# Optimization experiments

Hardware: AMD Instinct MI355X
Metric: run time of the kernel (lower is better)

The kernel has to match this reference:

```python
import jax, jax.numpy as jnp
import numpy as np

NUM_NODES = 50000
HIDDEN = 128
NUM_REL = 8
NUM_EDGES = 600000


def setup_inputs() -> dict:
    key = jax.random.key(0)
    ks = jax.random.split(key, 10)
    s = 1.0 / np.sqrt(HIDDEN)
    return {
        "edge_index": jax.random.randint(ks[0], (2, NUM_EDGES), 0, NUM_NODES, dtype=jnp.int32),
        "edge_type": jax.random.randint(ks[1], (NUM_EDGES,), 0, NUM_REL, dtype=jnp.int32),
        "node_emb": jax.random.normal(ks[2], (NUM_NODES, HIDDEN), jnp.float32),
        "W1": jax.random.normal(ks[3], (NUM_REL, HIDDEN, HIDDEN), jnp.float32) * s,
        "root1": jax.random.normal(ks[4], (HIDDEN, HIDDEN), jnp.float32) * s,
        "b1": jnp.zeros((HIDDEN,), jnp.float32),
        "W2": jax.random.normal(ks[5], (NUM_REL, HIDDEN, HIDDEN), jnp.float32) * s,
        "root2": jax.random.normal(ks[6], (HIDDEN, HIDDEN), jnp.float32) * s,
        "b2": jnp.zeros((HIDDEN,), jnp.float32),
    }


def rgcn_layer(x, W, root, bias, src, dst, rel):
    # PyG RGCNConv: per-relation MEAN aggregation of neighbor features,
    # transformed by relation weight, plus root transform and bias.
    N = x.shape[0]
    R = W.shape[0]
    # transform node features by every relation weight: [N, R, F]
    xw = jnp.einsum('nd,rdf->nrf', x, W)
    # per-(dst, relation) in-edge counts for mean normalization
    cnt = jnp.zeros((N, R), x.dtype).at[dst, rel].add(1.0)
    inv = 1.0 / jnp.maximum(cnt, 1.0)
    # per-edge message, normalized by destination's per-relation degree
    msg = xw[src, rel] * inv[dst, rel][:, None]  # [E, F]
    agg = jnp.zeros((N, W.shape[2]), x.dtype).at[dst].add(msg)
    return agg + x @ root + bias


def reference(edge_index, edge_type, node_emb, W1, root1, b1, W2, root2, b2):
    src, dst = edge_index[0], edge_index[1]
    h = jax.nn.relu(rgcn_layer(node_emb, W1, root1, b1, src, dst, edge_type))
    out = rgcn_layer(h, W2, root2, b2, src, dst, edge_type)
    return out
```

## Files before the change

### kernel.cpp

```cpp
#include <hip/hip_runtime.h>

#define H 128
#define RREL 8
#define NJ 9
#define MT 32
#define LROW 1160

typedef short bf16x8 __attribute__((ext_vector_type(8)));
typedef float f32x4 __attribute__((ext_vector_type(4)));
typedef unsigned short u16x8 __attribute__((ext_vector_type(8)));

static __device__ __forceinline__ unsigned short f2bf(float f) {
    unsigned int u = __float_as_uint(f);
    unsigned int r = (u + 0x7fffu + ((u >> 16) & 1u)) >> 16;
    return (unsigned short)r;
}
static __device__ __forceinline__ float bf2f(unsigned short u) {
    return __uint_as_float(((unsigned int)u) << 16);
}

__global__ void zero_kernel(int* p, long n) {
    long i = (long)blockIdx.x * blockDim.x + threadIdx.x;
    long stride = (long)gridDim.x * blockDim.x;
    for (; i < n; i += stride) p[i] = 0;
}

__global__ void count_kernel(const int* __restrict__ ei, const int* __restrict__ et,
                             int* __restrict__ cnt, int E) {
    int e = blockIdx.x * 256 + threadIdx.x;
    if (e >= E) return;
    int d = ei[E + e];
    int r = et[e];
    atomicAdd(&cnt[(size_t)d * RREL + r], 1);
}

__global__ void scan_block_kernel(const int* __restrict__ cnt, int* __restrict__ rploc,
                                  int* __restrict__ bsum, int N) {
    __shared__ int s[256];
    int t = threadIdx.x;
    int d = blockIdx.x * 256 + t;
    int v = 0;
    if (d < N) {
#pragma unroll
        for (int r = 0; r < RREL; ++r) v += cnt[(size_t)d * RREL + r];
    }
    s[t] = v;
    __syncthreads();
#pragma unroll
    for (int off = 1; off < 256; off <<= 1) {
        int u = 0;
        if (t >= off) u = s[t - off];
        __syncthreads();
        s[t] += u;
        __syncthreads();
    }
    if (d < N) rploc[d] = s[t] - v;
    if (t == 255) bsum[blockIdx.x] = s[255];
}

__global__ void finalize_kernel(const int* __restrict__ cnt, const int* __restrict__ rploc,
                                const int* __restrict__ bsum, int* __restrict__ rowptr,
                                int* __restrict__ rowptr2, float* __restrict__ inv,
                                int N, int nb) {
    __shared__ int s[256];
    int t = threadIdx.x;
    int v = (t < nb) ? bsum[t] : 0;
    s[t] = v;
    __syncthreads();
#pragma unroll
    for (int off = 1; off < 256; off <<= 1) {
        int u = 0;
        if (t >= off) u = s[t - off];
        __syncthreads();
        s[t] += u;
        __syncthreads();
    }
    int boffB = (blockIdx.x == 0) ? 0 : s[blockIdx.x - 1];
    int d = blockIdx.x * 256 + t;
    if (d >= N) return;
    int rp = rploc[d] + boffB;
    rowptr[d] = rp;
    int run = rp;
#pragma unroll
    for (int r = 0; r < RREL; ++r) {
        int c = cnt[(size_t)d * RREL + r];
        rowptr2[(size_t)d * RREL + r] = run;
        inv[(size_t)d * RREL + r] = 1.0f / (float)max(c, 1);
        run += c;
    }
    if (d == N - 1) rowptr[N] = run;
}

__global__ void fill_kernel(const int* __restrict__ ei, const int* __restrict__ et,
                            int* __restrict__ cursor, const int* __restrict__ rowptr2,
                            int* __restrict__ packed, int E) {
    int e = blockIdx.x * 256 + threadIdx.x;
    if (e >= E) return;
    int d = ei[E + e];
    int r = et[e];
    size_t bin = (size_t)d * RREL + r;
    int pos = rowptr2[bin] + atomicAdd(&cursor[bin], 1);
    packed[pos] = ei[e] | (r << 20);
}

__global__ void wcat_tobf_kernel(const float* __restrict__ W1, const float* __restrict__ r1,
                                 const float* __restrict__ W2, const float* __restrict__ r2,
                                 const float* __restrict__ b1, const float* __restrict__ b2,
                                 unsigned short* __restrict__ WTa1, unsigned short* __restrict__ WTa2,
                                 float* __restrict__ biasP,
                                 const float* __restrict__ x, unsigned short* __restrict__ xb,
                                 long nx) {
    const long per = (long)NJ * H * H;
    const long total = per + 2 * H + nx;
    for (long id = (long)blockIdx.x * 256 + threadIdx.x; id < total; id += (long)gridDim.x * 256) {
        if (id < per) {
            int j = (int)(id / (H * H));
            int fk = (int)(id - (long)j * (H * H));
            int f = fk >> 7, k = fk & 127;
            float v1 = (j < RREL) ? W1[((size_t)j * H + k) * H + f] : r1[(size_t)k * H + f];
            WTa1[id] = f2bf(v1);
            float v2 = (j < RREL) ? W2[((size_t)j * H + k) * H + f] : r2[(size_t)k * H + f];
            WTa2[id] = f2bf(v2);
        } else if (id < per + 2 * H) {
            int c = (int)(id - per);
            biasP[c] = (c < H) ? b1[c] : b2[c - H];
        } else {
            long i = id - per - 2 * H;
            xb[i] = f2bf(x[i]);
        }
    }
}

#define ACC(EE, XV, VV)                                                        \
    do {                                                                       \
        int r_ = ((VV) >> 20) & 7;                                             \
        bool nr_ = (r_ != rcur);                                               \
        float ivc_ = __shfl(ivl, gbase + r_);                                  \
        bool pr_ = (hb + (EE)) < m;                                            \
        u16x8 o_;                                                              \
        _Pragma("unroll")                                                      \
        for (int j = 0; j < 8; ++j) {                                          \
            float xx_ = bf2f((unsigned short)(XV)[j]);                         \
            float t0_ = nr_ ? 0.f : tmp[j];                                    \
            tmp[j] = t0_ + (pr_ ? xx_ : 0.f);                                  \
            o_[j] = f2bf(ivc_ * tmp[j]);                                       \
        }                                                                      \
        *(u16x8*)&rowp[r_ * H + kc] = o_;                                      \
        rcur = r_;                                                             \
    } while (0)

__global__ __launch_bounds__(512) void layer_kernel(const unsigned short* __restrict__ xin,
                                                    const unsigned short* __restrict__ WTa,
                                                    const float* __restrict__ biasP,
                                                    const float* __restrict__ inv,
                                                    const int* __restrict__ rowptr,
                                                    const int* __restrict__ packed,
                                                    float* __restrict__ outf,
                                                    unsigned short* __restrict__ outb,
                                                    int N, int relu) {
    __shared__ __align__(16) unsigned short aggS[MT * LROW];
    const int t = threadIdx.x;
    const int l = t & 63;
    const int w = t >> 6;
    const int g16 = t >> 4;
    const int fl = t & 15;
    const int kc = fl * 8;
    const int gbase = l & 48;
    const int Mbase = blockIdx.x * MT;
    const int d = Mbase + g16;
    const bool valid = d < N;

    unsigned short* rowp = &aggS[g16 * LROW];
    {
        u16x8 z = {0, 0, 0, 0, 0, 0, 0, 0};
#pragma unroll
        for (int c = 0; c < 8; ++c) *(u16x8*)&rowp[(c * 16 + fl) * 8] = z;
        if (valid) {
            *(u16x8*)&rowp[RREL * H + kc] = *(const u16x8*)&xin[(size_t)d * H + kc];
        } else {
            *(u16x8*)&rowp[RREL * H + kc] = z;
        }
    }

    int rp = 0;
    if (valid && fl < 2) rp = rowptr[d + fl];
    float ivl = 0.f;
    if (valid && fl < 8) ivl = inv[(size_t)d * RREL + fl];
    int beg = __shfl(rp, gbase);
    int end = __shfl(rp, gbase + 1);

    if (end > beg) {
        float tmp[8] = {};
        int rcur = 100;
        int idx0 = beg + fl; if (idx0 > end - 1) idx0 = end - 1;
        int pk = packed[idx0];
        for (int i = beg; i < end; i += 16) {
            int ni = i + 16 + fl; if (ni > end - 1) ni = end - 1;
            int pkN = packed[ni];
            int m = end - i;
            if (m > 16) m = 16;
#pragma unroll
            for (int half = 0; half < 2; ++half) {
                const int hb = half * 8;
                int v0 = __shfl(pk, gbase + hb + 0);
                int v1 = __shfl(pk, gbase + hb + 1);
                int v2 = __shfl(pk, gbase + hb + 2);
                int v3 = __shfl(pk, gbase + hb + 3);
                int v4 = __shfl(pk, gbase + hb + 4);
                int v5 = __shfl(pk, gbase + hb + 5);
                int v6 = __shfl(pk, gbase + hb + 6);
                int v7 = __shfl(pk, gbase + hb + 7);
                u16x8 x0 = *(const u16x8*)&xin[(size_t)(v0 & 0xFFFFF) * H + kc];
                u16x8 x1 = *(const u16x8*)&xin[(size_t)(v1 & 0xFFFFF) * H + kc];
                u16x8 x2 = *(const u16x8*)&xin[(size_t)(v2 & 0xFFFFF) * H + kc];
                u16x8 x3 = *(const u16x8*)&xin[(size_t)(v3 & 0xFFFFF) * H + kc];
                u16x8 x4 = *(const u16x8*)&xin[(size_t)(v4 & 0xFFFFF) * H + kc];
                u16x8 x5 = *(const u16x8*)&xin[(size_t)(v5 & 0xFFFFF) * H + kc];
                u16x8 x6 = *(const u16x8*)&xin[(size_t)(v6 & 0xFFFFF) * H + kc];
                u16x8 x7 = *(const u16x8*)&xin[(size_t)(v7 & 0xFFFFF) * H + kc];
                __builtin_amdgcn_sched_barrier(0);
                ACC(0, x0, v0);
                ACC(1, x1, v1);
                ACC(2, x2, v2);
                ACC(3, x3, v3);
                ACC(4, x4, v4);
                ACC(5, x5, v5);
                ACC(6, x6, v6);
                ACC(7, x7, v7);
            }
            pk = pkN;
        }
    }

    __syncthreads();

    const int colb = l & 15, quad = l >> 4;
    const int fcol = w * 16 + colb;
    const f32x4 fz = {0.f, 0.f, 0.f, 0.f};
    f32x4 acc0 = fz, acc1 = fz;
    const unsigned short* arow0 = &aggS[colb * LROW];
    const unsigned short* arow1 = &aggS[(16 + colb) * LROW];
#pragma unroll
    for (int j = 0; j < NJ; ++j) {
#pragma unroll
        for (int ks = 0; ks < 4; ++ks) {
            const int kl = ks * 32 + quad * 8;
            bf16x8 b = *(const bf16x8*)&WTa[((size_t)j * H + fcol) * H + kl];
            bf16x8 a0 = *(const bf16x8*)&arow0[j * H + kl];
            bf16x8 a1 = *(const bf16x8*)&arow1[j * H + kl];
            acc0 = __builtin_amdgcn_mfma_f32_16x16x32_bf16(a0, b, acc0, 0, 0, 0);
            acc1 = __builtin_amdgcn_mfma_f32_16x16x32_bf16(a1, b, acc1, 0, 0, 0);
        }
    }

    __syncthreads();
    float* stg = (float*)aggS;
    const float bcol = biasP[fcol];
#pragma unroll
    for (int i = 0; i < 4; ++i) {
        float v0 = acc0[i] + bcol;
        float v1 = acc1[i] + bcol;
        if (relu) { v0 = fmaxf(v0, 0.f); v1 = fmaxf(v1, 0.f); }
        stg[(quad * 4 + i) * 132 + fcol] = v0;
        stg[(16 + quad * 4 + i) * 132 + fcol] = v1;
    }
    __syncthreads();
    {
        int row = t >> 4;
        int dd = Mbase + row;
        if (dd < N) {
            int c0 = fl * 8;
            f32x4 p0 = *(const f32x4*)&stg[row * 132 + c0];
            f32x4 p1 = *(const f32x4*)&stg[row * 132 + c0 + 4];
            if (outf) {
                *(f32x4*)&outf[(size_t)dd * H + c0] = p0;
                *(f32x4*)&outf[(size_t)dd * H + c0 + 4] = p1;
            } else {
                u16x8 o;
#pragma unroll
                for (int j = 0; j < 4; ++j) { o[j] = f2bf(p0[j]); o[4 + j] = f2bf(p1[j]); }
                *(u16x8*)&outb[(size_t)dd * H + c0] = o;
            }
        }
    }
}

extern "C" void kernel_launch(void* const* d_in, const int* in_sizes, int n_in,
                              void* d_out, int out_size, void* d_ws, size_t ws_size,
                              hipStream_t stream) {
    const int* edge_index = (const int*)d_in[0];
    const int* edge_type  = (const int*)d_in[1];
    const float* node_emb = (const float*)d_in[2];
    const float* W1    = (const float*)d_in[3];
    const float* root1 = (const float*)d_in[4];
    const float* b1    = (const float*)d_in[5];
    const float* W2    = (const float*)d_in[6];
    const float* root2 = (const float*)d_in[7];
    const float* b2    = (const float*)d_in[8];
    float* out = (float*)d_out;

    const int E = in_sizes[1];
    const int N = in_sizes[2] / H;

    char* base = (char*)d_ws;
    size_t off = 0;
    auto take = [&](size_t bytes) { size_t o = off; off = (off + bytes + 63) & ~(size_t)63; return o; };
    int*   cnt     = (int*)  (base + take((size_t)N * RREL * 4));
    int*   cursor8 = (int*)  (base + take((size_t)N * RREL * 4));
    int*   rploc   = (int*)  (base + take((size_t)N * 4));
    int*   bsum    = (int*)  (base + take(256 * 4));
    int*   rowptr  = (int*)  (base + take(((size_t)N + 1) * 4));
    int*   rowptr2 = (int*)  (base + take((size_t)N * RREL * 4));
    float* inv     = (float*)(base + take((size_t)N * RREL * 4));
    int*   packed  = (int*)  (base + take((size_t)E * 4));
    unsigned short* WTa1 = (unsigned short*)(base + take((size_t)NJ * H * H * 2));
    unsigned short* WTa2 = (unsigned short*)(base + take((size_t)NJ * H * H * 2));
    float* biasP   = (float*)(base + take(2 * H * 4));
    unsigned short* xb  = (unsigned short*)(base + take((size_t)N * H * 2));
    unsigned short* hb  = (unsigned short*)(base + take((size_t)N * H * 2));
    (void)ws_size;

    const int nbScan = (N + 255) / 256;

    zero_kernel<<<512, 256, 0, stream>>>(cnt, (long)N * (2 * RREL));
    count_kernel<<<(E + 255) / 256, 256, 0, stream>>>(edge_index, edge_type, cnt, E);
    scan_block_kernel<<<nbScan, 256, 0, stream>>>(cnt, rploc, bsum, N);
    finalize_kernel<<<nbScan, 256, 0, stream>>>(cnt, rploc, bsum, rowptr, rowptr2, inv, N, nbScan);
    fill_kernel<<<(E + 255) / 256, 256, 0, stream>>>(edge_index, edge_type, cursor8, rowptr2, packed, E);
    wcat_tobf_kernel<<<2048, 256, 0, stream>>>(W1, root1, W2, root2, b1, b2,
                                               WTa1, WTa2, biasP, node_emb, xb, (long)N * H);

    const int gl = (N + MT - 1) / MT;
    layer_kernel<<<gl, 512, 0, stream>>>(xb, WTa1, biasP, inv, rowptr, packed,
                                         nullptr, hb, N, 1);
    layer_kernel<<<gl, 512, 0, stream>>>(hb, WTa2, biasP + H, inv, rowptr, packed,
                                         out, nullptr, N, 0);
}
```

Baseline: 339.7 us.

## Gather neighbors with one wavefront per destination row and register-pipelined loads

The aggregation phase now maps one full wavefront to each destination node (4 nodes per wave), with each lane handling 2 features, instead of 16 lanes per node with 8 features each. Packed edge entries are broadcast with readlane rather than shuffles. An 8-deep software pipeline of gather loads is kept in registers, and a relation's running sum is written to shared memory only when the relation changes, not after every edge. This cuts shuffle traffic and shared-memory stores, but each load is now a narrow 4-byte gather and nodes are processed serially within a wave, which may lower memory-level parallelism.

```diff
diff --git a/kernel.cpp b/kernel.cpp
--- a/kernel.cpp
+++ b/kernel.cpp
@@ -131,22 +131,36 @@
     }
 }
 
-#define ACC(EE, XV, VV)                                                        \
+#define FLUSH()                                                                \
     do {                                                                       \
-        int r_ = ((VV) >> 20) & 7;                                             \
-        bool nr_ = (r_ != rcur);                                               \
-        float ivc_ = __shfl(ivl, gbase + r_);                                  \
-        bool pr_ = (hb + (EE)) < m;                                            \
-        u16x8 o_;                                                              \
-        _Pragma("unroll")                                                      \
-        for (int j = 0; j < 8; ++j) {                                          \
-            float xx_ = bf2f((unsigned short)(XV)[j]);                         \
-            float t0_ = nr_ ? 0.f : tmp[j];                                    \
-            tmp[j] = t0_ + (pr_ ? xx_ : 0.f);                                  \
-            o_[j] = f2bf(ivc_ * tmp[j]);                                       \
+        if (rcur >= 0) {                                                       \
+            float iv_ = __shfl(ivv, rcur);                                     \
+            unsigned pw_ = ((unsigned)f2bf(a1 * iv_) << 16) |                  \
+                           (unsigned)f2bf(a0 * iv_);                           \
+            *(unsigned*)&rowp[rcur * H + c2] = pw_;                            \
         }                                                                      \
-        *(u16x8*)&rowp[r_ * H + kc] = o_;                                      \
-        rcur = r_;                                                             \
+    } while (0)
+
+#define PLD(S)                                                                 \
+    do {                                                                       \
+        int ec_ = (S) < cnt ? (S) : cnt - 1;                                   \
+        sv##S = __builtin_amdgcn_readlane(pkv, ec_);                           \
+        x##S = *(const unsigned*)&xin[(size_t)(sv##S & 0xFFFFF) * H + c2];     \
+    } while (0)
+
+#define RSTEP(S)                                                               \
+    do {                                                                       \
+        int e_ = e0 + (S);                                                     \
+        int r_ = (int)((sv##S >> 20) & 7);                                     \
+        if (r_ != rcur) { FLUSH(); rcur = r_; a0 = 0.f; a1 = 0.f; }            \
+        if (e_ < cnt) {                                                        \
+            a0 += __uint_as_float(x##S << 16);                                 \
+            a1 += __uint_as_float(x##S & 0xFFFF0000u);                         \
+        }                                                                      \
+        int en_ = e_ + 8;                                                      \
+        int ec_ = en_ < cnt ? en_ : cnt - 1;                                   \
+        sv##S = __builtin_amdgcn_readlane(pkv, ec_);                           \
+        x##S = *(const unsigned*)&xin[(size_t)(sv##S & 0xFFFFF) * H + c2];     \
     } while (0)
 
 __global__ __launch_bounds__(512) void layer_kernel(const unsigned short* __restrict__ xin,
@@ -161,81 +175,54 @@
     __shared__ __align__(16) unsigned short aggS[MT * LROW];
     const int t = threadIdx.x;
     const int l = t & 63;
-    const int w = t >> 6;
-    const int g16 = t >> 4;
-    const int fl = t & 15;
-    const int kc = fl * 8;
-    const int gbase = l & 48;
+    const int wu = __builtin_amdgcn_readfirstlane(t >> 6);
     const int Mbase = blockIdx.x * MT;
-    const int d = Mbase + g16;
-    const bool valid = d < N;
-
-    unsigned short* rowp = &aggS[g16 * LROW];
+
     {
+        const int g16 = t >> 4, fl = t & 15, kc = fl * 8;
+        const int d = Mbase + g16;
+        unsigned short* rowp0 = &aggS[g16 * LROW];
         u16x8 z = {0, 0, 0, 0, 0, 0, 0, 0};
 #pragma unroll
-        for (int c = 0; c < 8; ++c) *(u16x8*)&rowp[(c * 16 + fl) * 8] = z;
-        if (valid) {
-            *(u16x8*)&rowp[RREL * H + kc] = *(const u16x8*)&xin[(size_t)d * H + kc];
+        for (int c = 0; c < 8; ++c) *(u16x8*)&rowp0[(c * 16 + fl) * 8] = z;
+        if (d < N) {
+            *(u16x8*)&rowp0[RREL * H + kc] = *(const u16x8*)&xin[(size_t)d * H + kc];
         } else {
-            *(u16x8*)&rowp[RREL * H + kc] = z;
-        }
-    }
-
-    int rp = 0;
-    if (valid && fl < 2) rp = rowptr[d + fl];
-    float ivl = 0.f;
-    if (valid && fl < 8) ivl = inv[(size_t)d * RREL + fl];
-    int beg = __shfl(rp, gbase);
-    int end = __shfl(rp, gbase + 1);
-
-    if (end > beg) {
-        float tmp[8] = {};
-        int rcur = 100;
-        int idx0 = beg + fl; if (idx0 > end - 1) idx0 = end - 1;
-        int pk = packed[idx0];
-        for (int i = beg; i < end; i += 16) {
-            int ni = i + 16 + fl; if (ni > end - 1) ni = end - 1;
-            int pkN = packed[ni];
-            int m = end - i;
-            if (m > 16) m = 16;
-#pragma unroll
-            for (int half = 0; half < 2; ++half) {
-                const int hb = half * 8;
-                int v0 = __shfl(pk, gbase + hb + 0);
-                int v1 = __shfl(pk, gbase + hb + 1);
-                int v2 = __shfl(pk, gbase + hb + 2);
-                int v3 = __shfl(pk, gbase + hb + 3);
-                int v4 = __shfl(pk, gbase + hb + 4);
-                int v5 = __shfl(pk, gbase + hb + 5);
-                int v6 = __shfl(pk, gbase + hb + 6);
-                int v7 = __shfl(pk, gbase + hb + 7);
-                u16x8 x0 = *(const u16x8*)&xin[(size_t)(v0 & 0xFFFFF) * H + kc];
-                u16x8 x1 = *(const u16x8*)&xin[(size_t)(v1 & 0xFFFFF) * H + kc];
-                u16x8 x2 = *(const u16x8*)&xin[(size_t)(v2 & 0xFFFFF) * H + kc];
-                u16x8 x3 = *(const u16x8*)&xin[(size_t)(v3 & 0xFFFFF) * H + kc];
-                u16x8 x4 = *(const u16x8*)&xin[(size_t)(v4 & 0xFFFFF) * H + kc];
-                u16x8 x5 = *(const u16x8*)&xin[(size_t)(v5 & 0xFFFFF) * H + kc];
-                u16x8 x6 = *(const u16x8*)&xin[(size_t)(v6 & 0xFFFFF) * H + kc];
-                u16x8 x7 = *(const u16x8*)&xin[(size_t)(v7 & 0xFFFFF) * H + kc];
-                __builtin_amdgcn_sched_barrier(0);
-                ACC(0, x0, v0);
-                ACC(1, x1, v1);
-                ACC(2, x2, v2);
-                ACC(3, x3, v3);
-                ACC(4, x4, v4);
-                ACC(5, x5, v5);
-                ACC(6, x6, v6);
-                ACC(7, x7, v7);
+            *(u16x8*)&rowp0[RREL * H + kc] = z;
+        }
+    }
+
+    const int c2 = l * 2;
+    for (int q = 0; q < 4; ++q) {
+        const int dl = wu * 4 + q;
+        const int d = Mbase + dl;
+        if (d >= N) break;
+        const int beg = rowptr[d];
+        const int end = rowptr[d + 1];
+        if (end <= beg) continue;
+        const float ivv = inv[(size_t)d * RREL + (l & 7)];
+        unsigned short* rowp = &aggS[dl * LROW];
+        float a0 = 0.f, a1 = 0.f;
+        int rcur = -1;
+        for (int base = beg; base < end; base += 64) {
+            int cnt = end - base; if (cnt > 64) cnt = 64;
+            int pidx = base + l; if (pidx > end - 1) pidx = end - 1;
+            const int pkv = packed[pidx];
+            unsigned sv0, sv1, sv2, sv3, sv4, sv5, sv6, sv7;
+            unsigned x0, x1, x2, x3, x4, x5, x6, x7;
+            PLD(0); PLD(1); PLD(2); PLD(3); PLD(4); PLD(5); PLD(6); PLD(7);
+            for (int e0 = 0; e0 < cnt; e0 += 8) {
+                RSTEP(0); RSTEP(1); RSTEP(2); RSTEP(3);
+                RSTEP(4); RSTEP(5); RSTEP(6); RSTEP(7);
             }
-            pk = pkN;
-        }
+        }
+        FLUSH();
     }
 
     __syncthreads();
 
     const int colb = l & 15, quad = l >> 4;
-    const int fcol = w * 16 + colb;
+    const int fcol = wu * 16 + colb;
     const f32x4 fz = {0.f, 0.f, 0.f, 0.f};
     f32x4 acc0 = fz, acc1 = fz;
     const unsigned short* arow0 = &aggS[colb * LROW];
@@ -246,10 +233,10 @@
         for (int ks = 0; ks < 4; ++ks) {
             const int kl = ks * 32 + quad * 8;
             bf16x8 b = *(const bf16x8*)&WTa[((size_t)j * H + fcol) * H + kl];
-            bf16x8 a0 = *(const bf16x8*)&arow0[j * H + kl];
-            bf16x8 a1 = *(const bf16x8*)&arow1[j * H + kl];
-            acc0 = __builtin_amdgcn_mfma_f32_16x16x32_bf16(a0, b, acc0, 0, 0, 0);
-            acc1 = __builtin_amdgcn_mfma_f32_16x16x32_bf16(a1, b, acc1, 0, 0, 0);
+            bf16x8 a0f = *(const bf16x8*)&arow0[j * H + kl];
+            bf16x8 a1f = *(const bf16x8*)&arow1[j * H + kl];
+            acc0 = __builtin_amdgcn_mfma_f32_16x16x32_bf16(a0f, b, acc0, 0, 0, 0);
+            acc1 = __builtin_amdgcn_mfma_f32_16x16x32_bf16(a1f, b, acc1, 0, 0, 0);
         }
     }
 
@@ -267,6 +254,7 @@
     __syncthreads();
     {
         int row = t >> 4;
+        int fl = t & 15;
         int dd = Mbase + row;
         if (dd < N) {
             int c0 = fl * 8;
```

After: 356.3 us. 4.9% more time.

## Fuse all stages into one persistent cooperative kernel with grid syncs

Applied to the files above, without the earlier changes.

Replaces the eight separate launches (zero, count, scan, finalize, fill, weight/feature conversion, two layers) with a single cooperative persistent kernel that uses grid-wide barriers between phases. The CSR fill now decrements the count array instead of using a separate cursor array, which drops one zeroing pass. The layer phases pull tiles through an atomic work counter. This removes launch gaps, at the cost of grid.sync overhead and a grid capped at occupancy (at most 512 blocks), which may limit parallelism in the atomic and streaming phases.

```diff
diff --git a/kernel.cpp b/kernel.cpp
--- a/kernel.cpp
+++ b/kernel.cpp
@@ -1,4 +1,7 @@
 #include <hip/hip_runtime.h>
+#include <hip/hip_cooperative_groups.h>
+
+namespace cg = cooperative_groups;
 
 #define H 128
 #define RREL 8
@@ -19,117 +22,17 @@
     return __uint_as_float(((unsigned int)u) << 16);
 }
 
-__global__ void zero_kernel(int* p, long n) {
-    long i = (long)blockIdx.x * blockDim.x + threadIdx.x;
-    long stride = (long)gridDim.x * blockDim.x;
-    for (; i < n; i += stride) p[i] = 0;
-}
-
-__global__ void count_kernel(const int* __restrict__ ei, const int* __restrict__ et,
-                             int* __restrict__ cnt, int E) {
-    int e = blockIdx.x * 256 + threadIdx.x;
-    if (e >= E) return;
-    int d = ei[E + e];
-    int r = et[e];
-    atomicAdd(&cnt[(size_t)d * RREL + r], 1);
-}
-
-__global__ void scan_block_kernel(const int* __restrict__ cnt, int* __restrict__ rploc,
-                                  int* __restrict__ bsum, int N) {
-    __shared__ int s[256];
-    int t = threadIdx.x;
-    int d = blockIdx.x * 256 + t;
-    int v = 0;
-    if (d < N) {
-#pragma unroll
-        for (int r = 0; r < RREL; ++r) v += cnt[(size_t)d * RREL + r];
-    }
-    s[t] = v;
-    __syncthreads();
-#pragma unroll
-    for (int off = 1; off < 256; off <<= 1) {
-        int u = 0;
-        if (t >= off) u = s[t - off];
-        __syncthreads();
-        s[t] += u;
-        __syncthreads();
-    }
-    if (d < N) rploc[d] = s[t] - v;
-    if (t == 255) bsum[blockIdx.x] = s[255];
-}
-
-__global__ void finalize_kernel(const int* __restrict__ cnt, const int* __restrict__ rploc,
-                                const int* __restrict__ bsum, int* __restrict__ rowptr,
-                                int* __restrict__ rowptr2, float* __restrict__ inv,
-                                int N, int nb) {
-    __shared__ int s[256];
-    int t = threadIdx.x;
-    int v = (t < nb) ? bsum[t] : 0;
-    s[t] = v;
-    __syncthreads();
-#pragma unroll
-    for (int off = 1; off < 256; off <<= 1) {
-        int u = 0;
-        if (t >= off) u = s[t - off];
-        __syncthreads();
-        s[t] += u;
-        __syncthreads();
-    }
-    int boffB = (blockIdx.x == 0) ? 0 : s[blockIdx.x - 1];
-    int d = blockIdx.x * 256 + t;
-    if (d >= N) return;
-    int rp = rploc[d] + boffB;
-    rowptr[d] = rp;
-    int run = rp;
-#pragma unroll
-    for (int r = 0; r < RREL; ++r) {
-        int c = cnt[(size_t)d * RREL + r];
-        rowptr2[(size_t)d * RREL + r] = run;
-        inv[(size_t)d * RREL + r] = 1.0f / (float)max(c, 1);
-        run += c;
-    }
-    if (d == N - 1) rowptr[N] = run;
-}
-
-__global__ void fill_kernel(const int* __restrict__ ei, const int* __restrict__ et,
-                            int* __restrict__ cursor, const int* __restrict__ rowptr2,
-                            int* __restrict__ packed, int E) {
-    int e = blockIdx.x * 256 + threadIdx.x;
-    if (e >= E) return;
-    int d = ei[E + e];
-    int r = et[e];
-    size_t bin = (size_t)d * RREL + r;
-    int pos = rowptr2[bin] + atomicAdd(&cursor[bin], 1);
-    packed[pos] = ei[e] | (r << 20);
-}
-
-__global__ void wcat_tobf_kernel(const float* __restrict__ W1, const float* __restrict__ r1,
-                                 const float* __restrict__ W2, const float* __restrict__ r2,
-                                 const float* __restrict__ b1, const float* __restrict__ b2,
-                                 unsigned short* __restrict__ WTa1, unsigned short* __restrict__ WTa2,
-                                 float* __restrict__ biasP,
-                                 const float* __restrict__ x, unsigned short* __restrict__ xb,
-                                 long nx) {
-    const long per = (long)NJ * H * H;
-    const long total = per + 2 * H + nx;
-    for (long id = (long)blockIdx.x * 256 + threadIdx.x; id < total; id += (long)gridDim.x * 256) {
-        if (id < per) {
-            int j = (int)(id / (H * H));
-            int fk = (int)(id - (long)j * (H * H));
-            int f = fk >> 7, k = fk & 127;
-            float v1 = (j < RREL) ? W1[((size_t)j * H + k) * H + f] : r1[(size_t)k * H + f];
-            WTa1[id] = f2bf(v1);
-            float v2 = (j < RREL) ? W2[((size_t)j * H + k) * H + f] : r2[(size_t)k * H + f];
-            WTa2[id] = f2bf(v2);
-        } else if (id < per + 2 * H) {
-            int c = (int)(id - per);
-            biasP[c] = (c < H) ? b1[c] : b2[c - H];
-        } else {
-            long i = id - per - 2 * H;
-            xb[i] = f2bf(x[i]);
-        }
-    }
-}
+struct Args {
+    const int* ei; const int* et; const float* x;
+    const float* W1; const float* r1; const float* b1;
+    const float* W2; const float* r2; const float* b2;
+    float* out;
+    int* cnt; int* rploc; int* bsum; int* ctr;
+    int* rowptr; int* rowptr2; float* inv; int* packed;
+    unsigned short* WTa1; unsigned short* WTa2; float* biasP;
+    unsigned short* xb; unsigned short* hb;
+    int N; int E; int ntiles; int nchunk;
+};
 
 #define ACC(EE, XV, VV)                                                        \
     do {                                                                       \
@@ -149,16 +52,11 @@
         rcur = r_;                                                             \
     } while (0)
 
-__global__ __launch_bounds__(512) void layer_kernel(const unsigned short* __restrict__ xin,
-                                                    const unsigned short* __restrict__ WTa,
-                                                    const float* __restrict__ biasP,
-                                                    const float* __restrict__ inv,
-                                                    const int* __restrict__ rowptr,
-                                                    const int* __restrict__ packed,
-                                                    float* __restrict__ outf,
-                                                    unsigned short* __restrict__ outb,
-                                                    int N, int relu) {
-    __shared__ __align__(16) unsigned short aggS[MT * LROW];
+static __device__ void layer_tile(unsigned short* aggS, const unsigned short* xin,
+                                  const unsigned short* WTa, const float* biasP,
+                                  const float* inv, const int* rowptr, const int* packed,
+                                  float* outf, unsigned short* outb,
+                                  int N, int relu, int tile) {
     const int t = threadIdx.x;
     const int l = t & 63;
     const int w = t >> 6;
@@ -166,7 +64,7 @@
     const int fl = t & 15;
     const int kc = fl * 8;
     const int gbase = l & 48;
-    const int Mbase = blockIdx.x * MT;
+    const int Mbase = tile * MT;
     const int d = Mbase + g16;
     const bool valid = d < N;
 
@@ -285,54 +183,190 @@
     }
 }
 
+__global__ __launch_bounds__(512) void mega_kernel(Args a) {
+    __shared__ __align__(16) unsigned short smem[MT * LROW];
+    __shared__ int tileS;
+    cg::grid_group grid = cg::this_grid();
+    const int t = threadIdx.x;
+    const int bid = blockIdx.x;
+    const int nb = gridDim.x;
+    const long gid = (long)bid * 512 + t;
+    const long gsz = (long)nb * 512;
+
+    if (gid == 0) { a.ctr[0] = 0; a.ctr[1] = 0; }
+    for (long i = gid; i < (long)a.N * RREL; i += gsz) a.cnt[i] = 0;
+    {
+        const long per = (long)NJ * H * H;
+        const long total = per + 2 * H + (long)a.N * H;
+        for (long id = gid; id < total; id += gsz) {
+            if (id < per) {
+                int j = (int)(id / (H * H));
+                int fk = (int)(id - (long)j * (H * H));
+                int f = fk >> 7, k = fk & 127;
+                float v1 = (j < RREL) ? a.W1[((size_t)j * H + k) * H + f] : a.r1[(size_t)k * H + f];
+                a.WTa1[id] = f2bf(v1);
+                float v2 = (j < RREL) ? a.W2[((size_t)j * H + k) * H + f] : a.r2[(size_t)k * H + f];
+                a.WTa2[id] = f2bf(v2);
+            } else if (id < per + 2 * H) {
+                int c = (int)(id - per);
+                a.biasP[c] = (c < H) ? a.b1[c] : a.b2[c - H];
+            } else {
+                long i2 = id - per - 2 * H;
+                a.xb[i2] = f2bf(a.x[i2]);
+            }
+        }
+    }
+    grid.sync();
+
+    for (long e = gid; e < a.E; e += gsz) {
+        int d = a.ei[a.E + e], r = a.et[e];
+        atomicAdd(&a.cnt[(size_t)d * RREL + r], 1);
+    }
+    grid.sync();
+
+    int* sS = (int*)smem;
+    for (int c = bid; c < a.nchunk; c += nb) {
+        int d = c * 512 + t;
+        int v = 0;
+        if (d < a.N) {
+#pragma unroll
+            for (int r = 0; r < RREL; ++r) v += a.cnt[(size_t)d * RREL + r];
+        }
+        sS[t] = v;
+        __syncthreads();
+#pragma unroll
+        for (int off = 1; off < 512; off <<= 1) {
+            int u = 0;
+            if (t >= off) u = sS[t - off];
+            __syncthreads();
+            sS[t] += u;
+            __syncthreads();
+        }
+        if (d < a.N) a.rploc[d] = sS[t] - v;
+        if (t == 511) a.bsum[c] = sS[511];
+        __syncthreads();
+    }
+    grid.sync();
+
+    {
+        int v = (t < a.nchunk) ? a.bsum[t] : 0;
+        sS[t] = v;
+        __syncthreads();
+#pragma unroll
+        for (int off = 1; off < 512; off <<= 1) {
+            int u = 0;
+            if (t >= off) u = sS[t - off];
+            __syncthreads();
+            sS[t] += u;
+            __syncthreads();
+        }
+        for (int c = bid; c < a.nchunk; c += nb) {
+            int boffB = (c == 0) ? 0 : sS[c - 1];
+            int d = c * 512 + t;
+            if (d < a.N) {
+                int rp = a.rploc[d] + boffB;
+                a.rowptr[d] = rp;
+                int run = rp;
+#pragma unroll
+                for (int r = 0; r < RREL; ++r) {
+                    int cc = a.cnt[(size_t)d * RREL + r];
+                    a.rowptr2[(size_t)d * RREL + r] = run;
+                    a.inv[(size_t)d * RREL + r] = 1.0f / (float)max(cc, 1);
+                    run += cc;
+                }
+                if (d == a.N - 1) a.rowptr[a.N] = run;
+            }
+        }
+    }
+    grid.sync();
+
+    for (long e = gid; e < a.E; e += gsz) {
+        int d = a.ei[a.E + e], r = a.et[e];
+        size_t bin = (size_t)d * RREL + r;
+        int old = atomicSub(&a.cnt[bin], 1);
+        a.packed[a.rowptr2[bin] + old - 1] = a.ei[e] | (r << 20);
+    }
+    grid.sync();
+
+    for (;;) {
+        if (t == 0) tileS = atomicAdd(&a.ctr[0], 1);
+        __syncthreads();
+        int tile = tileS;
+        if (tile >= a.ntiles) break;
+        layer_tile(smem, a.xb, a.WTa1, a.biasP, a.inv, a.rowptr, a.packed,
+                   nullptr, a.hb, a.N, 1, tile);
+        __syncthreads();
+    }
+    grid.sync();
+
+    for (;;) {
+        if (t == 0) tileS = atomicAdd(&a.ctr[1], 1);
+        __syncthreads();
+        int tile = tileS;
+        if (tile >= a.ntiles) break;
+        layer_tile(smem, a.hb, a.WTa2, a.biasP + H, a.inv, a.rowptr, a.packed,
+                   a.out, nullptr, a.N, 0, tile);
+        __syncthreads();
+    }
+}
+
 extern "C" void kernel_launch(void* const* d_in, const int* in_sizes, int n_in,
                               void* d_out, int out_size, void* d_ws, size_t ws_size,
                               hipStream_t stream) {
-    const int* edge_index = (const int*)d_in[0];
-    const int* edge_type  = (const int*)d_in[1];
-    const float* node_emb = (const float*)d_in[2];
-    const float* W1    = (const float*)d_in[3];
-    const float* root1 = (const float*)d_in[4];
-    const float* b1    = (const float*)d_in[5];
-    const float* W2    = (const float*)d_in[6];
-    const float* root2 = (const float*)d_in[7];
-    const float* b2    = (const float*)d_in[8];
-    float* out = (float*)d_out;
-
     const int E = in_sizes[1];
     const int N = in_sizes[2] / H;
 
     char* base = (char*)d_ws;
     size_t off = 0;
     auto take = [&](size_t bytes) { size_t o = off; off = (off + bytes + 63) & ~(size_t)63; return o; };
-    int*   cnt     = (int*)  (base + take((size_t)N * RREL * 4));
-    int*   cursor8 = (int*)  (base + take((size_t)N * RREL * 4));
-    int*   rploc   = (int*)  (base + take((size_t)N * 4));
-    int*   bsum    = (int*)  (base + take(256 * 4));
-    int*   rowptr  = (int*)  (base + take(((size_t)N + 1) * 4));
-    int*   rowptr2 = (int*)  (base + take((size_t)N * RREL * 4));
-    float* inv     = (float*)(base + take((size_t)N * RREL * 4));
-    int*   packed  = (int*)  (base + take((size_t)E * 4));
-    unsigned short* WTa1 = (unsigned short*)(base + take((size_t)NJ * H * H * 2));
-    unsigned short* WTa2 = (unsigned short*)(base + take((size_t)NJ * H * H * 2));
-    float* biasP   = (float*)(base + take(2 * H * 4));
-    unsigned short* xb  = (unsigned short*)(base + take((size_t)N * H * 2));
-    unsigned short* hb  = (unsigned short*)(base + take((size_t)N * H * 2));
+
+    Args a;
+    a.ei = (const int*)d_in[0];
+    a.et = (const int*)d_in[1];
+    a.x  = (const float*)d_in[2];
+    a.W1 = (const float*)d_in[3];
+    a.r1 = (const float*)d_in[4];
+    a.b1 = (const float*)d_in[5];
+    a.W2 = (const float*)d_in[6];
+    a.r2 = (const float*)d_in[7];
+    a.b2 = (const float*)d_in[8];
+    a.out = (float*)d_out;
+
+    a.cnt     = (int*)  (base + take((size_t)N * RREL * 4));
+    a.rploc   = (int*)  (base + take((size_t)N * 4));
+    a.bsum    = (int*)  (base + take(512 * 4));
+    a.ctr     = (int*)  (base + take(2 * 4));
+    a.rowptr  = (int*)  (base + take(((size_t)N + 1) * 4));
+    a.rowptr2 = (int*)  (base + take((size_t)N * RREL * 4));
+    a.inv     = (float*)(base + take((size_t)N * RREL * 4));
+    a.packed  = (int*)  (base + take((size_t)E * 4));
+    a.WTa1    = (unsigned short*)(base + take((size_t)NJ * H * H * 2));
+    a.WTa2    = (unsigned short*)(base + take((size_t)NJ * H * H * 2));
+    a.biasP   = (float*)(base + take(2 * H * 4));
+    a.xb      = (unsigned short*)(base + take((size_t)N * H * 2));
+    a.hb      = (unsigned short*)(base + take((size_t)N * H * 2));
     (void)ws_size;
 
-    const int nbScan = (N + 255) / 256;
-
-    zero_kernel<<<512, 256, 0, stream>>>(cnt, (long)N * (2 * RREL));
-    count_kernel<<<(E + 255) / 256, 256, 0, stream>>>(edge_index, edge_type, cnt, E);
-    scan_block_kernel<<<nbScan, 256, 0, stream>>>(cnt, rploc, bsum, N);
-    finalize_kernel<<<nbScan, 256, 0, stream>>>(cnt, rploc, bsum, rowptr, rowptr2, inv, N, nbScan);
-    fill_kernel<<<(E + 255) / 256, 256, 0, stream>>>(edge_index, edge_type, cursor8, rowptr2, packed, E);
-    wcat_tobf_kernel<<<2048, 256, 0, stream>>>(W1, root1, W2, root2, b1, b2,
-                                               WTa1, WTa2, biasP, node_emb, xb, (long)N * H);
-
-    const int gl = (N + MT - 1) / MT;
-    layer_kernel<<<gl, 512, 0, stream>>>(xb, WTa1, biasP, inv, rowptr, packed,
-                                         nullptr, hb, N, 1);
-    layer_kernel<<<gl, 512, 0, stream>>>(hb, WTa2, biasP + H, inv, rowptr, packed,
-                                         out, nullptr, N, 0);
-}
+    a.N = N;
+    a.E = E;
+    a.ntiles = (N + MT - 1) / MT;
+    a.nchunk = (N + 511) / 512;
+
+    static int g_grid = 0;
+    if (g_grid == 0) {
+        int occ = 0;
+        (void)hipOccupancyMaxActiveBlocksPerMultiprocessor(&occ, mega_kernel, 512, 0);
+        int dev = 0, ncu = 256;
+        if (hipGetDevice(&dev) == hipSuccess) {
+            hipDeviceProp_t prop;
+            if (hipGetDeviceProperties(&prop, dev) == hipSuccess) ncu = prop.multiProcessorCount;
+        }
+        if (occ < 1) occ = 1;
+        long cap = (long)occ * ncu;
+        g_grid = (int)(cap < 512 ? cap : 512);
+        if (g_grid < 1) g_grid = 1;
+    }
+
+    void* params[] = {(void*)&a};
+    hipLaunchCooperativeKernel((void*)mega_kernel, dim3(g_grid), dim3(512), params, 0, stream);
+}
```

Measured after the change: 620.6 us. +82.7%, slower.
